# Performance work log

Measured on AMD Instinct MI355X. Metric: run time of the kernel, lower is better.

## Reference

```python
import jax, jax.numpy as jnp
import numpy as np

DIM = 64
HEADS = 8
DIM_HEAD = 64
INNER = HEADS * DIM_HEAD  # 512
FB, HB, WB = 3, 4, 4
Q_L = HB * WB            # 16
KV_L = FB * HB * WB      # 48
EPS = 1e-5


def conv3(x, W):
    # x: [N,Cin,H,W], W: [Cout,Cin,3,3], stride 1, pad 1, no bias
    return jax.lax.conv_general_dilated(
        x, W, window_strides=(1, 1), padding='SAME',
        dimension_numbers=('NCHW', 'OIHW', 'NCHW'))


def layernorm(x, g, b):
    # normalize over last (channel) dim, matching nn.LayerNorm(dim)
    mu = jnp.mean(x, axis=-1, keepdims=True)
    var = jnp.mean(jnp.square(x - mu), axis=-1, keepdims=True)
    return (x - mu) * jax.lax.rsqrt(var + EPS) * g + b


def warp_nearest(x, flow):
    # Faithful to flow_warp-style grid_sample(mode='nearest', padding='zeros',
    # align_corners=True): sample x at round(grid + flow), zeros out-of-range.
    n, c, h, w = x.shape
    gy, gx = jnp.meshgrid(jnp.arange(h, dtype=x.dtype),
                          jnp.arange(w, dtype=x.dtype), indexing='ij')
    px = gx[None] + flow[:, 0]  # [n,h,w]
    py = gy[None] + flow[:, 1]
    ix = jnp.round(px).astype(jnp.int32)
    iy = jnp.round(py).astype(jnp.int32)
    valid = (ix >= 0) & (ix < w) & (iy >= 0) & (iy < h)
    flat = jnp.clip(iy, 0, h - 1) * w + jnp.clip(ix, 0, w - 1)  # [n,h,w]

    def gather_one(xi, fi):
        return jnp.take(xi.reshape(c, h * w), fi.reshape(-1), axis=1).reshape(c, h, w)

    out = jax.vmap(gather_one)(x, flat)
    return out * valid[:, None].astype(x.dtype)


def setup_inputs() -> dict:
    key = jax.random.key(0)
    ks = jax.random.split(key, 12)
    b, h, w = 2, 128, 128
    inp = {
        'q_inp': jax.random.normal(ks[0], (b, 1, DIM, h, w), jnp.float32),
        'k_inp': jax.random.normal(ks[1], (b, 3, DIM, h, w), jnp.float32),
        'flow_f': jax.random.normal(ks[2], (b, 2, h, w), jnp.float32) * 4.0,
        'flow_b': jax.random.normal(ks[3], (b, 2, h, w), jnp.float32) * 4.0,
        'gq': jnp.ones((DIM,), jnp.float32),
        'bq': jnp.zeros((DIM,), jnp.float32),
        'gkv': jnp.ones((DIM,), jnp.float32),
        'bkv': jnp.zeros((DIM,), jnp.float32),
        'Wq': jax.random.normal(ks[4], (INNER, DIM, 3, 3), jnp.float32) * 0.02,
        'Wkv': jax.random.normal(ks[5], (2 * INNER, DIM, 3, 3), jnp.float32) * 0.02,
        'Wout': jax.random.normal(ks[6], (DIM, INNER, 3, 3), jnp.float32) * 0.02,
        'static_a': jax.random.truncated_normal(ks[7], -2.0, 2.0, (1, HEADS, Q_L, KV_L), jnp.float32),
    }
    return inp


def _fgsw_msa(q_inp, k_inp, flow_f, flow_b, gq, bq, gkv, bkv, Wq, Wkv, Wout, static_a):
    b, f_q, c, h, w = q_inp.shape
    # flow-guided warp of forward/backward key frames (nearest, zeros padding)
    k_f = warp_nearest(k_inp[:, 0], flow_f)
    k_r = k_inp[:, 1]
    k_b = warp_nearest(k_inp[:, 2], flow_b)
    k_stack = jnp.stack([k_f, k_r, k_b], axis=1)  # [b,3,c,h,w]

    # LayerNorm over channels
    qn = layernorm(q_inp.transpose(0, 1, 3, 4, 2), gq, bq).transpose(0, 1, 4, 2, 3)
    kvn = layernorm(k_stack.transpose(0, 1, 3, 4, 2), gkv, bkv).transpose(0, 1, 4, 2, 3)

    # conv QKV projections
    q = conv3(qn.reshape(b * f_q, c, h, w), Wq)       # [b, INNER, h, w]
    kv = conv3(kvn.reshape(b * 3, c, h, w), Wkv)      # [3b, 2*INNER, h, w]
    k, v = jnp.split(kv, 2, axis=1)

    nh, nw = h // HB, w // WB

    def part(t, f):
        # [(b f), C, H, W] -> [(b nh nw), heads, f*HB*WB, d]
        C = t.shape[1]
        t = t.reshape(b, f, C, nh, HB, nw, WB)
        t = t.transpose(0, 3, 5, 1, 4, 6, 2)  # b, nh, nw, f, p1, p2, C
        t = t.reshape(b * nh * nw, f * HB * WB, HEADS, C // HEADS)
        return t.transpose(0, 2, 1, 3)

    qh = part(q, f_q) * (DIM_HEAD ** -0.5)
    kh = part(k, 3)
    vh = part(v, 3)

    sim = jnp.einsum('bhid,bhjd->bhij', qh, kh) + static_a
    attn = jax.nn.softmax(sim, axis=-1)
    out = jnp.einsum('bhij,bhjd->bhid', attn, vh)  # [(b nh nw), heads, Q_L, d]

    out = out.transpose(0, 2, 1, 3).reshape(b * nh * nw, f_q * HB * WB, INNER)
    out = out.reshape(b, nh, nw, f_q, HB, WB, INNER)
    out = out.transpose(0, 3, 6, 1, 4, 2, 5).reshape(b * f_q, INNER, h, w)
    out = conv3(out, Wout).reshape(b, f_q, c, h, w)
    return out


def reference(q_inp, k_inp, flow_f, flow_b, gq, bq, gkv, bkv, Wq, Wkv, Wout, static_a):
    return _fgsw_msa(q_inp, k_inp, flow_f, flow_b, gq, bq, gkv, bkv, Wq, Wkv, Wout, static_a)
```

## Files before the change

kernel.cpp:

```cpp
#include <hip/hip_runtime.h>


typedef __attribute__((ext_vector_type(8))) short bf16x8;
typedef __attribute__((ext_vector_type(4))) float f32x4;

__device__ __forceinline__ float bs2f(unsigned short s) {
    return __uint_as_float(((unsigned int)s) << 16);
}
__device__ __forceinline__ unsigned short f2bs(float f) {
    unsigned int u = __float_as_uint(f);
    u += 0x7fffu + ((u >> 16) & 1u);
    return (unsigned short)(u >> 16);
}

__global__ __launch_bounds__(256) void ln_q_kernel(
    const float* __restrict__ q_inp, const float* __restrict__ g,
    const float* __restrict__ b, unsigned short* __restrict__ qn)
{
    int wid  = (blockIdx.x * 256 + threadIdx.x) >> 6;
    int lane = threadIdx.x & 63;
    int pix  = wid & 16383;
    int bb   = wid >> 14;
    float val = q_inp[(bb * 64 + lane) * 16384 + pix];
    float s = val;
    #pragma unroll
    for (int m = 1; m < 64; m <<= 1) s += __shfl_xor(s, m);
    float mu = s * (1.f / 64.f);
    float d = val - mu;
    float s2 = d * d;
    #pragma unroll
    for (int m = 1; m < 64; m <<= 1) s2 += __shfl_xor(s2, m);
    float o = d * rsqrtf(s2 * (1.f / 64.f) + 1e-5f) * g[lane] + b[lane];
    qn[wid * 64 + lane] = f2bs(o);
}

__global__ __launch_bounds__(256) void warp_ln_kv_kernel(
    const float* __restrict__ k_inp, const float* __restrict__ flow_f,
    const float* __restrict__ flow_b, const float* __restrict__ g,
    const float* __restrict__ b, unsigned short* __restrict__ kvn)
{
    int wid  = (blockIdx.x * 256 + threadIdx.x) >> 6;
    int lane = threadIdx.x & 63;
    int x  = wid & 127;
    int y  = (wid >> 7) & 127;
    int bf = wid >> 14;
    int f  = bf % 3, bb = bf / 3;
    float val;
    if (f == 1) {
        val = k_inp[(bf * 64 + lane) * 16384 + y * 128 + x];
    } else {
        const float* fl = (f == 0) ? flow_f : flow_b;
        float fx = fl[(bb * 2 + 0) * 16384 + y * 128 + x];
        float fy = fl[(bb * 2 + 1) * 16384 + y * 128 + x];
        int ix = (int)rintf((float)x + fx);
        int iy = (int)rintf((float)y + fy);
        if (ix >= 0 && ix < 128 && iy >= 0 && iy < 128)
            val = k_inp[(bf * 64 + lane) * 16384 + iy * 128 + ix];
        else
            val = 0.f;
    }
    float s = val;
    #pragma unroll
    for (int m = 1; m < 64; m <<= 1) s += __shfl_xor(s, m);
    float mu = s * (1.f / 64.f);
    float d = val - mu;
    float s2 = d * d;
    #pragma unroll
    for (int m = 1; m < 64; m <<= 1) s2 += __shfl_xor(s2, m);
    float o = d * rsqrtf(s2 * (1.f / 64.f) + 1e-5f) * g[lane] + b[lane];
    kvn[wid * 64 + lane] = f2bs(o);
}

__global__ __launch_bounds__(256) void repack_bf16_kernel(
    const float* __restrict__ w, unsigned short* __restrict__ wp,
    int IC, int total)
{
    int idx = blockIdx.x * 256 + threadIdx.x;
    if (idx >= total) return;
    int tap = idx % 9;
    int tmp = idx / 9;
    int ic  = tmp % IC;
    int oc  = tmp / IC;
    wp[oc * IC * 9 + (ic >> 6) * 576 + tap * 64 + (ic & 63)] = f2bs(w[idx]);
}

__global__ __launch_bounds__(256) void fused_attn_kernel(
    const unsigned short* __restrict__ qn,
    const unsigned short* __restrict__ kvn,
    const unsigned short* __restrict__ wq,
    const unsigned short* __restrict__ wkv,
    const float* __restrict__ sa,
    unsigned short* __restrict__ ao)
{
    __shared__ __align__(16) unsigned char smem[50624];
    unsigned short* kvp   = (unsigned short*)smem;
    unsigned short* qls   = (unsigned short*)(smem + 15552);
    unsigned short* kls   = (unsigned short*)(smem + 32192);
    unsigned short* vls_T = (unsigned short*)(smem + 39104);
    unsigned short* pls   = (unsigned short*)(smem + 48320);
    unsigned short* qpatch = kls;

    const int tid  = threadIdx.x;
    const int lane = tid & 63;
    const int w    = tid >> 6;
    const int wx = blockIdx.x & 31, wy = blockIdx.x >> 5;
    const int bb = blockIdx.y;
    const int gx0 = wx * 4 - 1, gy0 = wy * 4 - 1;

    for (int u = tid; u < 864; u += 256) {
        int f = u / 288, rest = u - f * 288;
        int pos = rest >> 3, seg = rest & 7;
        int hy = pos / 6, hx = pos - hy * 6;
        int gy = gy0 + hy, gx = gx0 + hx;
        uint4 v = make_uint4(0u, 0u, 0u, 0u);
        if ((unsigned)gy < 128u && (unsigned)gx < 128u)
            v = *reinterpret_cast<const uint4*>(
                kvn + (((bb * 3 + f) * 128 + gy) * 128 + gx) * 64 + seg * 8);
        *reinterpret_cast<uint4*>(kvp + (f * 36 + pos) * 72 + seg * 8) = v;
    }
    for (int u = tid; u < 288; u += 256) {
        int pos = u >> 3, seg = u & 7;
        int hy = pos / 6, hx = pos - hy * 6;
        int gy = gy0 + hy, gx = gx0 + hx;
        uint4 v = make_uint4(0u, 0u, 0u, 0u);
        if ((unsigned)gy < 128u && (unsigned)gx < 128u)
            v = *reinterpret_cast<const uint4*>(
                qn + ((bb * 128 + gy) * 128 + gx) * 64 + seg * 8);
        *reinterpret_cast<uint4*>(qpatch + pos * 72 + seg * 8) = v;
    }
    for (int u = tid; u < 1024; u += 256) {
        int row = u >> 4, c = 48 + (u & 15);
        vls_T[row * 72 + c] = 0;
    }
    if (tid < 256) {
        int row = tid >> 4, c = 48 + (tid & 15);
        pls[row * 72 + c] = 0;
    }
    __syncthreads();

    const int r  = lane & 15;
    const int kg = lane >> 4;
    const int py = r >> 2, px = r & 3;

    for (int g = 0; g < 2; ++g) {
        f32x4 acc0 = {0.f,0.f,0.f,0.f}, acc1 = acc0, acc2 = acc0, acc3 = acc0;
        #pragma unroll 3
        for (int kk = 0; kk < 18; ++kk) {
            int tap = kk >> 1, ic0 = (kk & 1) * 32;
            int ky = tap / 3, kx = tap - ky * 3;
            int pos = (py + ky) * 6 + (px + kx);
            bf16x8 a = *reinterpret_cast<const bf16x8*>(qpatch + pos * 72 + ic0 + kg * 8);
            const unsigned short* wb = wq + (w * 8 + g * 4) * 16 * 576 + kk * 32 + kg * 8;
            bf16x8 b0 = *reinterpret_cast<const bf16x8*>(wb + (0 * 16 + r) * 576);
            bf16x8 b1 = *reinterpret_cast<const bf16x8*>(wb + (1 * 16 + r) * 576);
            bf16x8 b2 = *reinterpret_cast<const bf16x8*>(wb + (2 * 16 + r) * 576);
            bf16x8 b3 = *reinterpret_cast<const bf16x8*>(wb + (3 * 16 + r) * 576);
            acc0 = __builtin_amdgcn_mfma_f32_16x16x32_bf16(a, b0, acc0, 0, 0, 0);
            acc1 = __builtin_amdgcn_mfma_f32_16x16x32_bf16(a, b1, acc1, 0, 0, 0);
            acc2 = __builtin_amdgcn_mfma_f32_16x16x32_bf16(a, b2, acc2, 0, 0, 0);
            acc3 = __builtin_amdgcn_mfma_f32_16x16x32_bf16(a, b3, acc3, 0, 0, 0);
        }
        #pragma unroll
        for (int reg = 0; reg < 4; ++reg) {
            int row = kg * 4 + reg;
            int cb  = (w * 8 + g * 4) * 16 + r;
            qls[row * 520 + cb +  0] = f2bs(0.125f * acc0[reg]);
            qls[row * 520 + cb + 16] = f2bs(0.125f * acc1[reg]);
            qls[row * 520 + cb + 32] = f2bs(0.125f * acc2[reg]);
            qls[row * 520 + cb + 48] = f2bs(0.125f * acc3[reg]);
        }
    }
    __syncthreads();

    const int is_v = w >> 1, pair = w & 1;
    const int si = tid >> 4, sjg = tid & 15;

    for (int h = 0; h < 8; ++h) {
        {
            f32x4 c00 = {0.f,0.f,0.f,0.f}, c01 = c00, c10 = c00, c11 = c00, c20 = c00, c21 = c00;
            #pragma unroll 3
            for (int kk = 0; kk < 18; ++kk) {
                int tap = kk >> 1, ic0 = (kk & 1) * 32;
                int ky = tap / 3, kx = tap - ky * 3;
                int pos = (py + ky) * 6 + (px + kx);
                bf16x8 a0 = *reinterpret_cast<const bf16x8*>(kvp + pos * 72 + ic0 + kg * 8);
                bf16x8 a1 = *reinterpret_cast<const bf16x8*>(kvp + (36 + pos) * 72 + ic0 + kg * 8);
                bf16x8 a2 = *reinterpret_cast<const bf16x8*>(kvp + (72 + pos) * 72 + ic0 + kg * 8);
                int ocb = is_v * 512 + h * 64 + pair * 32;
                const unsigned short* wb = wkv + (size_t)ocb * 576 + kk * 32 + kg * 8;
                bf16x8 b0 = *reinterpret_cast<const bf16x8*>(wb + (size_t)(r) * 576);
                bf16x8 b1 = *reinterpret_cast<const bf16x8*>(wb + (size_t)(16 + r) * 576);
                c00 = __builtin_amdgcn_mfma_f32_16x16x32_bf16(a0, b0, c00, 0, 0, 0);
                c10 = __builtin_amdgcn_mfma_f32_16x16x32_bf16(a1, b0, c10, 0, 0, 0);
                c20 = __builtin_amdgcn_mfma_f32_16x16x32_bf16(a2, b0, c20, 0, 0, 0);
                c01 = __builtin_amdgcn_mfma_f32_16x16x32_bf16(a0, b1, c01, 0, 0, 0);
                c11 = __builtin_amdgcn_mfma_f32_16x16x32_bf16(a1, b1, c11, 0, 0, 0);
                c21 = __builtin_amdgcn_mfma_f32_16x16x32_bf16(a2, b1, c21, 0, 0, 0);
            }
            if (!is_v) {
                #pragma unroll
                for (int reg = 0; reg < 4; ++reg) {
                    int jr = kg * 4 + reg;
                    int cb = pair * 32 + r;
                    kls[(jr +  0) * 72 + cb]      = f2bs(c00[reg]);
                    kls[(jr + 16) * 72 + cb]      = f2bs(c10[reg]);
                    kls[(jr + 32) * 72 + cb]      = f2bs(c20[reg]);
                    kls[(jr +  0) * 72 + cb + 16] = f2bs(c01[reg]);
                    kls[(jr + 16) * 72 + cb + 16] = f2bs(c11[reg]);
                    kls[(jr + 32) * 72 + cb + 16] = f2bs(c21[reg]);
                }
            } else {
                #pragma unroll
                for (int reg = 0; reg < 4; ++reg) {
                    int jr = kg * 4 + reg;
                    int d0 = pair * 32 + r;
                    vls_T[d0 * 72        + jr]      = f2bs(c00[reg]);
                    vls_T[d0 * 72        + 16 + jr] = f2bs(c10[reg]);
                    vls_T[d0 * 72        + 32 + jr] = f2bs(c20[reg]);
                    vls_T[(d0 + 16) * 72 + jr]      = f2bs(c01[reg]);
                    vls_T[(d0 + 16) * 72 + 16 + jr] = f2bs(c11[reg]);
                    vls_T[(d0 + 16) * 72 + 32 + jr] = f2bs(c21[reg]);
                }
            }
        }
        __syncthreads();

        if (w < 3) {
            f32x4 s_acc = {0.f, 0.f, 0.f, 0.f};
            #pragma unroll
            for (int s = 0; s < 2; ++s) {
                bf16x8 a = *reinterpret_cast<const bf16x8*>(
                    qls + r * 520 + h * 64 + s * 32 + kg * 8);
                bf16x8 b = *reinterpret_cast<const bf16x8*>(
                    kls + (w * 16 + r) * 72 + s * 32 + kg * 8);
                s_acc = __builtin_amdgcn_mfma_f32_16x16x32_bf16(a, b, s_acc, 0, 0, 0);
            }
            #pragma unroll
            for (int reg = 0; reg < 4; ++reg) {
                int i = kg * 4 + reg, j = w * 16 + r;
                float val = s_acc[reg] + sa[(h * 16 + i) * 48 + j];
                pls[i * 72 + j] = f2bs(val);
            }
        }
        __syncthreads();

        {
            float p0 = bs2f(pls[si * 72 + sjg]);
            float p1 = bs2f(pls[si * 72 + sjg + 16]);
            float p2 = bs2f(pls[si * 72 + sjg + 32]);
            float mx = fmaxf(p0, fmaxf(p1, p2));
            #pragma unroll
            for (int m = 1; m < 16; m <<= 1) mx = fmaxf(mx, __shfl_xor(mx, m));
            p0 = __expf(p0 - mx); p1 = __expf(p1 - mx); p2 = __expf(p2 - mx);
            float sum = p0 + p1 + p2;
            #pragma unroll
            for (int m = 1; m < 16; m <<= 1) sum += __shfl_xor(sum, m);
            float inv = 1.f / sum;
            pls[si * 72 + sjg]      = f2bs(p0 * inv);
            pls[si * 72 + sjg + 16] = f2bs(p1 * inv);
            pls[si * 72 + sjg + 32] = f2bs(p2 * inv);
        }
        __syncthreads();

        {
            f32x4 o_acc = {0.f, 0.f, 0.f, 0.f};
            #pragma unroll
            for (int s = 0; s < 2; ++s) {
                bf16x8 a = *reinterpret_cast<const bf16x8*>(
                    pls + r * 72 + s * 32 + kg * 8);
                bf16x8 b = *reinterpret_cast<const bf16x8*>(
                    vls_T + (w * 16 + r) * 72 + s * 32 + kg * 8);
                o_acc = __builtin_amdgcn_mfma_f32_16x16x32_bf16(a, b, o_acc, 0, 0, 0);
            }
            #pragma unroll
            for (int reg = 0; reg < 4; ++reg) {
                int i = kg * 4 + reg;
                int y = wy * 4 + (i >> 2), x = wx * 4 + (i & 3);
                ao[((bb * 128 + y) * 128 + x) * 512 + h * 64 + w * 16 + r] = f2bs(o_acc[reg]);
            }
        }
        __syncthreads();
    }
}

__global__ __launch_bounds__(256) void conv512_kernel(
    const unsigned short* __restrict__ in,
    const unsigned short* __restrict__ wp,
    float* __restrict__ out)
{
    __shared__ __align__(16) unsigned short patch[100 * 72];
    const int tid = threadIdx.x, lane = tid & 63, w = tid >> 6;
    const int tx = blockIdx.x & 15, ty = blockIdx.x >> 4;
    const int img = blockIdx.y;
    const int gx0 = tx * 8 - 1, gy0 = ty * 8 - 1;
    const int r = lane & 15, kg = lane >> 4;

    f32x4 acc0 = {0.f,0.f,0.f,0.f}, acc1 = acc0, acc2 = acc0, acc3 = acc0;

    for (int ci = 0; ci < 8; ++ci) {
        __syncthreads();
        for (int u = tid; u < 800; u += 256) {
            int pos = u >> 3, seg = u & 7;
            int hy = pos / 10, hx = pos - hy * 10;
            int gy = gy0 + hy, gx = gx0 + hx;
            uint4 v = make_uint4(0u, 0u, 0u, 0u);
            if ((unsigned)gy < 128u && (unsigned)gx < 128u)
                v = *reinterpret_cast<const uint4*>(
                    in + (((size_t)img * 128 + gy) * 128 + gx) * 512 + ci * 64 + seg * 8);
            *reinterpret_cast<uint4*>(patch + pos * 72 + seg * 8) = v;
        }
        __syncthreads();
        #pragma unroll 3
        for (int kk = 0; kk < 18; ++kk) {
            int tap = kk >> 1, ic0 = (kk & 1) * 32;
            int ky = tap / 3, kx = tap - ky * 3;
            int oc = w * 16 + r;
            bf16x8 b = *reinterpret_cast<const bf16x8*>(
                wp + (size_t)oc * 4608 + ci * 576 + kk * 32 + kg * 8);
            #pragma unroll
            for (int m = 0; m < 4; ++m) {
                int rr = m * 16 + r;
                int pos = ((rr >> 3) + ky) * 10 + (rr & 7) + kx;
                bf16x8 a = *reinterpret_cast<const bf16x8*>(patch + pos * 72 + ic0 + kg * 8);
                f32x4& acc = (m == 0) ? acc0 : (m == 1) ? acc1 : (m == 2) ? acc2 : acc3;
                acc = __builtin_amdgcn_mfma_f32_16x16x32_bf16(a, b, acc, 0, 0, 0);
            }
        }
    }
    const int oc = w * 16 + r;
    #pragma unroll
    for (int m = 0; m < 4; ++m) {
        const f32x4& acc = (m == 0) ? acc0 : (m == 1) ? acc1 : (m == 2) ? acc2 : acc3;
        int r0 = m * 16 + kg * 4;
        int gy = ty * 8 + (r0 >> 3), gx = tx * 8 + (r0 & 7);
        *reinterpret_cast<float4*>(
            out + (((size_t)img * 64 + oc) * 128 + gy) * 128 + gx) =
            make_float4(acc[0], acc[1], acc[2], acc[3]);
    }
}

extern "C" void kernel_launch(void* const* d_in, const int* in_sizes, int n_in,
                              void* d_out, int out_size, void* d_ws, size_t ws_size,
                              hipStream_t stream)
{
    const float* q_inp  = (const float*)d_in[0];
    const float* k_inp  = (const float*)d_in[1];
    const float* flow_f = (const float*)d_in[2];
    const float* flow_b = (const float*)d_in[3];
    const float* gq     = (const float*)d_in[4];
    const float* bq     = (const float*)d_in[5];
    const float* gkv    = (const float*)d_in[6];
    const float* bkv    = (const float*)d_in[7];
    const float* Wq     = (const float*)d_in[8];
    const float* Wkv    = (const float*)d_in[9];
    const float* Wout   = (const float*)d_in[10];
    const float* sa     = (const float*)d_in[11];

    if (ws_size < 55050240u) return;

    char* ws = (char*)d_ws;
    unsigned short* qn   = (unsigned short*)(ws + 0);
    unsigned short* kvn  = (unsigned short*)(ws + 4194304);
    unsigned short* ao   = (unsigned short*)(ws + 16777216);
    unsigned short* wqb  = (unsigned short*)(ws + 50331648);
    unsigned short* wkvb = (unsigned short*)(ws + 50921472);
    unsigned short* wopb = (unsigned short*)(ws + 52101120);

    ln_q_kernel<<<8192, 256, 0, stream>>>(q_inp, gq, bq, qn);
    warp_ln_kv_kernel<<<24576, 256, 0, stream>>>(k_inp, flow_f, flow_b, gkv, bkv, kvn);

    repack_bf16_kernel<<<1152, 256, 0, stream>>>(Wq,   wqb,  64,  294912);
    repack_bf16_kernel<<<2304, 256, 0, stream>>>(Wkv,  wkvb, 64,  589824);
    repack_bf16_kernel<<<1152, 256, 0, stream>>>(Wout, wopb, 512, 294912);

    fused_attn_kernel<<<dim3(1024, 2), 256, 0, stream>>>(qn, kvn, wqb, wkvb, sa, ao);

    conv512_kernel<<<dim3(256, 2), 256, 0, stream>>>(ao, wopb, (float*)d_out);
}
```

Measured before the change: 606.8 us.

## Split Q conv into separate kernel and fuse QK/softmax in registers

```diff
diff --git a/kernel.cpp b/kernel.cpp
--- a/kernel.cpp
+++ b/kernel.cpp
@@ -84,21 +84,71 @@
     wp[oc * IC * 9 + (ic >> 6) * 576 + tap * 64 + (ic & 63)] = f2bs(w[idx]);
 }
 
-__global__ __launch_bounds__(256) void fused_attn_kernel(
+__global__ __launch_bounds__(512) void qconv_kernel(
     const unsigned short* __restrict__ qn,
+    const unsigned short* __restrict__ wq,
+    unsigned short* __restrict__ qc)
+{
+    __shared__ __align__(16) unsigned short patch[100 * 80];
+    const int tid = threadIdx.x, lane = tid & 63, w = tid >> 6;
+    const int tx = blockIdx.x & 15, ty = blockIdx.x >> 4;
+    const int img = blockIdx.y;
+    const int gx0 = tx * 8 - 1, gy0 = ty * 8 - 1;
+    const int r = lane & 15, kg = lane >> 4;
+    const int m = w >> 1, nh = w & 1;
+
+    for (int u = tid; u < 800; u += 512) {
+        int pos = u >> 3, seg = u & 7;
+        int hy = pos / 10, hx = pos - hy * 10;
+        int gy = gy0 + hy, gx = gx0 + hx;
+        uint4 v = make_uint4(0u, 0u, 0u, 0u);
+        if ((unsigned)gy < 128u && (unsigned)gx < 128u)
+            v = *reinterpret_cast<const uint4*>(
+                qn + ((img * 128 + gy) * 128 + gx) * 64 + seg * 8);
+        *reinterpret_cast<uint4*>(patch + pos * 80 + seg * 8) = v;
+    }
+    __syncthreads();
+
+    f32x4 acc[16];
+    #pragma unroll
+    for (int n = 0; n < 16; ++n) acc[n] = f32x4{0.f, 0.f, 0.f, 0.f};
+
+    #pragma unroll 2
+    for (int kk = 0; kk < 18; ++kk) {
+        int tap = kk >> 1, ic0 = (kk & 1) * 32;
+        int ky = tap / 3, kx = tap - ky * 3;
+        int pos = (m * 2 + (r >> 3) + ky) * 10 + (r & 7) + kx;
+        bf16x8 a = *reinterpret_cast<const bf16x8*>(patch + pos * 80 + ic0 + kg * 8);
+        #pragma unroll
+        for (int n = 0; n < 16; ++n) {
+            bf16x8 b = *reinterpret_cast<const bf16x8*>(
+                wq + (size_t)(nh * 256 + n * 16 + r) * 576 + kk * 32 + kg * 8);
+            acc[n] = __builtin_amdgcn_mfma_f32_16x16x32_bf16(a, b, acc[n], 0, 0, 0);
+        }
+    }
+    #pragma unroll
+    for (int n = 0; n < 16; ++n) {
+        #pragma unroll
+        for (int reg = 0; reg < 4; ++reg) {
+            int p = m * 16 + kg * 4 + reg;
+            int y = ty * 8 + (p >> 3), x = tx * 8 + (p & 7);
+            qc[((size_t)(img * 128 + y) * 128 + x) * 512 + nh * 256 + n * 16 + r] =
+                f2bs(0.125f * acc[n][reg]);
+        }
+    }
+}
+
+__global__ __launch_bounds__(256, 4) void fused_attn_kernel(
     const unsigned short* __restrict__ kvn,
-    const unsigned short* __restrict__ wq,
     const unsigned short* __restrict__ wkv,
     const float* __restrict__ sa,
-    unsigned short* __restrict__ ao)
-{
-    __shared__ __align__(16) unsigned char smem[50624];
+    unsigned short* __restrict__ qcao)
+{
+    __shared__ __align__(16) unsigned char smem[35712];
     unsigned short* kvp   = (unsigned short*)smem;
-    unsigned short* qls   = (unsigned short*)(smem + 15552);
-    unsigned short* kls   = (unsigned short*)(smem + 32192);
-    unsigned short* vls_T = (unsigned short*)(smem + 39104);
-    unsigned short* pls   = (unsigned short*)(smem + 48320);
-    unsigned short* qpatch = kls;
+    unsigned short* kls   = (unsigned short*)(smem + 17280);
+    unsigned short* vls_T = (unsigned short*)(smem + 24192);
+    unsigned short* pls   = (unsigned short*)(smem + 33408);
 
     const int tid  = threadIdx.x;
     const int lane = tid & 63;
@@ -116,23 +166,13 @@
         if ((unsigned)gy < 128u && (unsigned)gx < 128u)
             v = *reinterpret_cast<const uint4*>(
                 kvn + (((bb * 3 + f) * 128 + gy) * 128 + gx) * 64 + seg * 8);
-        *reinterpret_cast<uint4*>(kvp + (f * 36 + pos) * 72 + seg * 8) = v;
-    }
-    for (int u = tid; u < 288; u += 256) {
-        int pos = u >> 3, seg = u & 7;
-        int hy = pos / 6, hx = pos - hy * 6;
-        int gy = gy0 + hy, gx = gx0 + hx;
-        uint4 v = make_uint4(0u, 0u, 0u, 0u);
-        if ((unsigned)gy < 128u && (unsigned)gx < 128u)
-            v = *reinterpret_cast<const uint4*>(
-                qn + ((bb * 128 + gy) * 128 + gx) * 64 + seg * 8);
-        *reinterpret_cast<uint4*>(qpatch + pos * 72 + seg * 8) = v;
+        *reinterpret_cast<uint4*>(kvp + (f * 36 + pos) * 80 + seg * 8) = v;
     }
     for (int u = tid; u < 1024; u += 256) {
         int row = u >> 4, c = 48 + (u & 15);
         vls_T[row * 72 + c] = 0;
     }
-    if (tid < 256) {
+    {
         int row = tid >> 4, c = 48 + (tid & 15);
         pls[row * 72 + c] = 0;
     }
@@ -141,55 +181,43 @@
     const int r  = lane & 15;
     const int kg = lane >> 4;
     const int py = r >> 2, px = r & 3;
-
-    for (int g = 0; g < 2; ++g) {
-        f32x4 acc0 = {0.f,0.f,0.f,0.f}, acc1 = acc0, acc2 = acc0, acc3 = acc0;
-        #pragma unroll 3
-        for (int kk = 0; kk < 18; ++kk) {
-            int tap = kk >> 1, ic0 = (kk & 1) * 32;
-            int ky = tap / 3, kx = tap - ky * 3;
-            int pos = (py + ky) * 6 + (px + kx);
-            bf16x8 a = *reinterpret_cast<const bf16x8*>(qpatch + pos * 72 + ic0 + kg * 8);
-            const unsigned short* wb = wq + (w * 8 + g * 4) * 16 * 576 + kk * 32 + kg * 8;
-            bf16x8 b0 = *reinterpret_cast<const bf16x8*>(wb + (0 * 16 + r) * 576);
-            bf16x8 b1 = *reinterpret_cast<const bf16x8*>(wb + (1 * 16 + r) * 576);
-            bf16x8 b2 = *reinterpret_cast<const bf16x8*>(wb + (2 * 16 + r) * 576);
-            bf16x8 b3 = *reinterpret_cast<const bf16x8*>(wb + (3 * 16 + r) * 576);
-            acc0 = __builtin_amdgcn_mfma_f32_16x16x32_bf16(a, b0, acc0, 0, 0, 0);
-            acc1 = __builtin_amdgcn_mfma_f32_16x16x32_bf16(a, b1, acc1, 0, 0, 0);
-            acc2 = __builtin_amdgcn_mfma_f32_16x16x32_bf16(a, b2, acc2, 0, 0, 0);
-            acc3 = __builtin_amdgcn_mfma_f32_16x16x32_bf16(a, b3, acc3, 0, 0, 0);
-        }
-        #pragma unroll
-        for (int reg = 0; reg < 4; ++reg) {
-            int row = kg * 4 + reg;
-            int cb  = (w * 8 + g * 4) * 16 + r;
-            qls[row * 520 + cb +  0] = f2bs(0.125f * acc0[reg]);
-            qls[row * 520 + cb + 16] = f2bs(0.125f * acc1[reg]);
-            qls[row * 520 + cb + 32] = f2bs(0.125f * acc2[reg]);
-            qls[row * 520 + cb + 48] = f2bs(0.125f * acc3[reg]);
-        }
-    }
-    __syncthreads();
-
     const int is_v = w >> 1, pair = w & 1;
-    const int si = tid >> 4, sjg = tid & 15;
+
+    const unsigned short* qbase =
+        qcao + ((size_t)(bb * 128 + wy * 4 + (r >> 2)) * 128 + wx * 4 + (r & 3)) * 512;
+
+    f32x4 oacc = {0.f, 0.f, 0.f, 0.f};
 
     for (int h = 0; h < 8; ++h) {
+        if (h > 0) {
+            #pragma unroll
+            for (int reg = 0; reg < 4; ++reg) {
+                int i = kg * 4 + reg;
+                int y = wy * 4 + (i >> 2), x = wx * 4 + (i & 3);
+                qcao[((size_t)(bb * 128 + y) * 128 + x) * 512 + (h - 1) * 64 + w * 16 + r] =
+                    f2bs(oacc[reg]);
+            }
+        }
+
         {
+            const int ocb = is_v * 512 + h * 64 + pair * 32;
+            const unsigned short* wb = wkv + (size_t)ocb * 576 + kg * 8;
+            bf16x8 nb0 = *reinterpret_cast<const bf16x8*>(wb + (size_t)r * 576);
+            bf16x8 nb1 = *reinterpret_cast<const bf16x8*>(wb + (size_t)(16 + r) * 576);
             f32x4 c00 = {0.f,0.f,0.f,0.f}, c01 = c00, c10 = c00, c11 = c00, c20 = c00, c21 = c00;
-            #pragma unroll 3
+            #pragma unroll 2
             for (int kk = 0; kk < 18; ++kk) {
+                bf16x8 b0 = nb0, b1 = nb1;
+                if (kk < 17) {
+                    nb0 = *reinterpret_cast<const bf16x8*>(wb + (size_t)r * 576 + (kk + 1) * 32);
+                    nb1 = *reinterpret_cast<const bf16x8*>(wb + (size_t)(16 + r) * 576 + (kk + 1) * 32);
+                }
                 int tap = kk >> 1, ic0 = (kk & 1) * 32;
                 int ky = tap / 3, kx = tap - ky * 3;
                 int pos = (py + ky) * 6 + (px + kx);
-                bf16x8 a0 = *reinterpret_cast<const bf16x8*>(kvp + pos * 72 + ic0 + kg * 8);
-                bf16x8 a1 = *reinterpret_cast<const bf16x8*>(kvp + (36 + pos) * 72 + ic0 + kg * 8);
-                bf16x8 a2 = *reinterpret_cast<const bf16x8*>(kvp + (72 + pos) * 72 + ic0 + kg * 8);
-                int ocb = is_v * 512 + h * 64 + pair * 32;
-                const unsigned short* wb = wkv + (size_t)ocb * 576 + kk * 32 + kg * 8;
-                bf16x8 b0 = *reinterpret_cast<const bf16x8*>(wb + (size_t)(r) * 576);
-                bf16x8 b1 = *reinterpret_cast<const bf16x8*>(wb + (size_t)(16 + r) * 576);
+                bf16x8 a0 = *reinterpret_cast<const bf16x8*>(kvp + pos * 80 + ic0 + kg * 8);
+                bf16x8 a1 = *reinterpret_cast<const bf16x8*>(kvp + (36 + pos) * 80 + ic0 + kg * 8);
+                bf16x8 a2 = *reinterpret_cast<const bf16x8*>(kvp + (72 + pos) * 80 + ic0 + kg * 8);
                 c00 = __builtin_amdgcn_mfma_f32_16x16x32_bf16(a0, b0, c00, 0, 0, 0);
                 c10 = __builtin_amdgcn_mfma_f32_16x16x32_bf16(a1, b0, c10, 0, 0, 0);
                 c20 = __builtin_amdgcn_mfma_f32_16x16x32_bf16(a2, b0, c20, 0, 0, 0);
@@ -225,61 +253,55 @@
         }
         __syncthreads();
 
-        if (w < 3) {
-            f32x4 s_acc = {0.f, 0.f, 0.f, 0.f};
+        {
+            bf16x8 qa0 = *reinterpret_cast<const bf16x8*>(qbase + h * 64 + kg * 8);
+            bf16x8 qa1 = *reinterpret_cast<const bf16x8*>(qbase + h * 64 + 32 + kg * 8);
+            f32x4 s0 = {0.f,0.f,0.f,0.f}, s1 = s0, s2 = s0;
             #pragma unroll
-            for (int s = 0; s < 2; ++s) {
-                bf16x8 a = *reinterpret_cast<const bf16x8*>(
-                    qls + r * 520 + h * 64 + s * 32 + kg * 8);
-                bf16x8 b = *reinterpret_cast<const bf16x8*>(
-                    kls + (w * 16 + r) * 72 + s * 32 + kg * 8);
-                s_acc = __builtin_amdgcn_mfma_f32_16x16x32_bf16(a, b, s_acc, 0, 0, 0);
-            }
-            #pragma unroll
-            for (int reg = 0; reg < 4; ++reg) {
-                int i = kg * 4 + reg, j = w * 16 + r;
-                float val = s_acc[reg] + sa[(h * 16 + i) * 48 + j];
-                pls[i * 72 + j] = f2bs(val);
-            }
-        }
-        __syncthreads();
-
-        {
-            float p0 = bs2f(pls[si * 72 + sjg]);
-            float p1 = bs2f(pls[si * 72 + sjg + 16]);
-            float p2 = bs2f(pls[si * 72 + sjg + 32]);
-            float mx = fmaxf(p0, fmaxf(p1, p2));
-            #pragma unroll
-            for (int m = 1; m < 16; m <<= 1) mx = fmaxf(mx, __shfl_xor(mx, m));
-            p0 = __expf(p0 - mx); p1 = __expf(p1 - mx); p2 = __expf(p2 - mx);
-            float sum = p0 + p1 + p2;
-            #pragma unroll
-            for (int m = 1; m < 16; m <<= 1) sum += __shfl_xor(sum, m);
-            float inv = 1.f / sum;
-            pls[si * 72 + sjg]      = f2bs(p0 * inv);
-            pls[si * 72 + sjg + 16] = f2bs(p1 * inv);
-            pls[si * 72 + sjg + 32] = f2bs(p2 * inv);
-        }
-        __syncthreads();
-
-        {
-            f32x4 o_acc = {0.f, 0.f, 0.f, 0.f};
-            #pragma unroll
-            for (int s = 0; s < 2; ++s) {
-                bf16x8 a = *reinterpret_cast<const bf16x8*>(
-                    pls + r * 72 + s * 32 + kg * 8);
-                bf16x8 b = *reinterpret_cast<const bf16x8*>(
-                    vls_T + (w * 16 + r) * 72 + s * 32 + kg * 8);
-                o_acc = __builtin_amdgcn_mfma_f32_16x16x32_bf16(a, b, o_acc, 0, 0, 0);
+            for (int t = 0; t < 3; ++t) {
+                bf16x8 b0 = *reinterpret_cast<const bf16x8*>(kls + (t * 16 + r) * 72 + kg * 8);
+                bf16x8 b1 = *reinterpret_cast<const bf16x8*>(kls + (t * 16 + r) * 72 + 32 + kg * 8);
+                f32x4& st = (t == 0) ? s0 : (t == 1) ? s1 : s2;
+                st = __builtin_amdgcn_mfma_f32_16x16x32_bf16(qa0, b0, st, 0, 0, 0);
+                st = __builtin_amdgcn_mfma_f32_16x16x32_bf16(qa1, b1, st, 0, 0, 0);
             }
             #pragma unroll
             for (int reg = 0; reg < 4; ++reg) {
                 int i = kg * 4 + reg;
-                int y = wy * 4 + (i >> 2), x = wx * 4 + (i & 3);
-                ao[((bb * 128 + y) * 128 + x) * 512 + h * 64 + w * 16 + r] = f2bs(o_acc[reg]);
-            }
+                float v0 = s0[reg] + sa[(h * 16 + i) * 48 + r];
+                float v1 = s1[reg] + sa[(h * 16 + i) * 48 + 16 + r];
+                float v2 = s2[reg] + sa[(h * 16 + i) * 48 + 32 + r];
+                float mx = fmaxf(v0, fmaxf(v1, v2));
+                #pragma unroll
+                for (int m = 1; m < 16; m <<= 1) mx = fmaxf(mx, __shfl_xor(mx, m));
+                float e0 = __expf(v0 - mx), e1 = __expf(v1 - mx), e2 = __expf(v2 - mx);
+                float sum = e0 + e1 + e2;
+                #pragma unroll
+                for (int m = 1; m < 16; m <<= 1) sum += __shfl_xor(sum, m);
+                float inv = 1.f / sum;
+                pls[i * 72 + r]      = f2bs(e0 * inv);
+                pls[i * 72 + 16 + r] = f2bs(e1 * inv);
+                pls[i * 72 + 32 + r] = f2bs(e2 * inv);
+            }
+        }
+
+        {
+            bf16x8 pa0 = *reinterpret_cast<const bf16x8*>(pls + r * 72 + kg * 8);
+            bf16x8 pa1 = *reinterpret_cast<const bf16x8*>(pls + r * 72 + 32 + kg * 8);
+            bf16x8 vb0 = *reinterpret_cast<const bf16x8*>(vls_T + (w * 16 + r) * 72 + kg * 8);
+            bf16x8 vb1 = *reinterpret_cast<const bf16x8*>(vls_T + (w * 16 + r) * 72 + 32 + kg * 8);
+            f32x4 o = {0.f, 0.f, 0.f, 0.f};
+            o = __builtin_amdgcn_mfma_f32_16x16x32_bf16(pa0, vb0, o, 0, 0, 0);
+            o = __builtin_amdgcn_mfma_f32_16x16x32_bf16(pa1, vb1, o, 0, 0, 0);
+            oacc = o;
         }
         __syncthreads();
+    }
+    #pragma unroll
+    for (int reg = 0; reg < 4; ++reg) {
+        int i = kg * 4 + reg;
+        int y = wy * 4 + (i >> 2), x = wx * 4 + (i & 3);
+        qcao[((size_t)(bb * 128 + y) * 128 + x) * 512 + 7 * 64 + w * 16 + r] = f2bs(oacc[reg]);
     }
 }
 
@@ -288,7 +310,7 @@
     const unsigned short* __restrict__ wp,
     float* __restrict__ out)
 {
-    __shared__ __align__(16) unsigned short patch[100 * 72];
+    __shared__ __align__(16) unsigned short patch[100 * 80];
     const int tid = threadIdx.x, lane = tid & 63, w = tid >> 6;
     const int tx = blockIdx.x & 15, ty = blockIdx.x >> 4;
     const int img = blockIdx.y;
@@ -307,7 +329,7 @@
             if ((unsigned)gy < 128u && (unsigned)gx < 128u)
                 v = *reinterpret_cast<const uint4*>(
                     in + (((size_t)img * 128 + gy) * 128 + gx) * 512 + ci * 64 + seg * 8);
-            *reinterpret_cast<uint4*>(patch + pos * 72 + seg * 8) = v;
+            *reinterpret_cast<uint4*>(patch + pos * 80 + seg * 8) = v;
         }
         __syncthreads();
         #pragma unroll 3
@@ -321,7 +343,7 @@
             for (int m = 0; m < 4; ++m) {
                 int rr = m * 16 + r;
                 int pos = ((rr >> 3) + ky) * 10 + (rr & 7) + kx;
-                bf16x8 a = *reinterpret_cast<const bf16x8*>(patch + pos * 72 + ic0 + kg * 8);
+                bf16x8 a = *reinterpret_cast<const bf16x8*>(patch + pos * 80 + ic0 + kg * 8);
                 f32x4& acc = (m == 0) ? acc0 : (m == 1) ? acc1 : (m == 2) ? acc2 : acc3;
                 acc = __builtin_amdgcn_mfma_f32_16x16x32_bf16(a, b, acc, 0, 0, 0);
             }
@@ -361,7 +383,7 @@
     char* ws = (char*)d_ws;
     unsigned short* qn   = (unsigned short*)(ws + 0);
     unsigned short* kvn  = (unsigned short*)(ws + 4194304);
-    unsigned short* ao   = (unsigned short*)(ws + 16777216);
+    unsigned short* qcao = (unsigned short*)(ws + 16777216);
     unsigned short* wqb  = (unsigned short*)(ws + 50331648);
     unsigned short* wkvb = (unsigned short*)(ws + 50921472);
     unsigned short* wopb = (unsigned short*)(ws + 52101120);
@@ -373,7 +395,9 @@
     repack_bf16_kernel<<<2304, 256, 0, stream>>>(Wkv,  wkvb, 64,  589824);
     repack_bf16_kernel<<<1152, 256, 0, stream>>>(Wout, wopb, 512, 294912);
 
-    fused_attn_kernel<<<dim3(1024, 2), 256, 0, stream>>>(qn, kvn, wqb, wkvb, sa, ao);
-
-    conv512_kernel<<<dim3(256, 2), 256, 0, stream>>>(ao, wopb, (float*)d_out);
-}
+    qconv_kernel<<<dim3(256, 2), 512, 0, stream>>>(qn, wqb, qcao);
+
+    fused_attn_kernel<<<dim3(1024, 2), 256, 0, stream>>>(kvn, wkvb, sa, qcao);
+
+    conv512_kernel<<<dim3(256, 2), 256, 0, stream>>>(qcao, wopb, (float*)d_out);
+}
```

Result: slower. 622.3 us (+2.6%).
